# Kernel optimization log

Hardware: AMD Instinct MI355X
Metric: run time of the kernel (lower is better)

The kernel has to match this reference:

```python
import jax, jax.numpy as jnp
import numpy as np

D_MODEL = 2048
N_HEADS = 32
N_KV = 8
HEAD_DIM = D_MODEL // N_HEADS  # 64
D_FF = 8192
ROPE_BASE = 10000.0
EPS = 1e-5
B, S = 2, 2048


def setup_inputs() -> dict:
    key = jax.random.key(0)
    ks = jax.random.split(key, 8)
    s = 0.02
    qkv_out = (N_HEADS + 2 * N_KV) * HEAD_DIM
    return {
        "x": jax.random.normal(ks[0], (B, S, D_MODEL), jnp.float32),
        "w_norm1": jnp.ones((D_MODEL,), jnp.float32),
        "w_qkv": jax.random.normal(ks[1], (D_MODEL, qkv_out), jnp.float32) * s,
        "w_out": jax.random.normal(ks[2], (D_MODEL, D_MODEL), jnp.float32) * s,
        "w_norm2": jnp.ones((D_MODEL,), jnp.float32),
        "w_gate": jax.random.normal(ks[3], (D_MODEL, D_FF), jnp.float32) * s,
        "w_up": jax.random.normal(ks[4], (D_MODEL, D_FF), jnp.float32) * s,
        "w_down": jax.random.normal(ks[5], (D_FF, D_MODEL), jnp.float32) * s,
    }


def _rmsnorm(x, w):
    var = jnp.mean(x * x, axis=-1, keepdims=True)
    return x * jax.lax.rsqrt(var + EPS) * w


def _rope(x, cos, sin):
    # x: [b, s, h, d]; cos/sin: [s, d/2]; non-interleaved (NeoX half split)
    half = x.shape[-1] // 2
    x1, x2 = x[..., :half], x[..., half:]
    c = cos[None, :, None, :]
    sn = sin[None, :, None, :]
    return jnp.concatenate([x1 * c - x2 * sn, x1 * sn + x2 * c], axis=-1)


def _forward(x, w_norm1, w_qkv, w_out, w_norm2, w_gate, w_up, w_down):
    b, s, d = x.shape
    # --- attention block ---
    h = _rmsnorm(x, w_norm1)
    qkv = h @ w_qkv  # [b, s, (H + 2*KV) * hd]
    q = qkv[..., : N_HEADS * HEAD_DIM].reshape(b, s, N_HEADS, HEAD_DIM)
    kv = qkv[..., N_HEADS * HEAD_DIM:].reshape(b, s, 2, N_KV, HEAD_DIM)
    k, v = kv[:, :, 0], kv[:, :, 1]

    inv_freq = 1.0 / (ROPE_BASE ** (jnp.arange(0, HEAD_DIM, 2, dtype=jnp.float32) / HEAD_DIM))
    t = jnp.arange(s, dtype=jnp.float32)
    freqs = t[:, None] * inv_freq[None, :]  # [s, hd/2]
    cos, sin = jnp.cos(freqs), jnp.sin(freqs)
    q = _rope(q, cos, sin)
    k = _rope(k, cos, sin)

    # GQA: repeat_interleave kv heads to match q heads
    g = N_HEADS // N_KV
    k = jnp.repeat(k, g, axis=2)  # [b, s, H, hd]
    v = jnp.repeat(v, g, axis=2)

    scale = 1.0 / np.sqrt(HEAD_DIM)
    scores = jnp.einsum("bqhd,bkhd->bhqk", q, k) * scale
    causal = jnp.tril(jnp.ones((s, s), bool))
    scores = jnp.where(causal[None, None], scores, jnp.finfo(scores.dtype).min)
    attn = jax.nn.softmax(scores, axis=-1)
    ctx = jnp.einsum("bhqk,bkhd->bqhd", attn, v).reshape(b, s, N_HEADS * HEAD_DIM)
    x = x + ctx @ w_out

    # --- MLP block (SwiGLU) ---
    h2 = _rmsnorm(x, w_norm2)
    mlp = (jax.nn.silu(h2 @ w_gate) * (h2 @ w_up)) @ w_down
    return x + mlp


def reference(x, w_norm1, w_qkv, w_out, w_norm2, w_gate, w_up, w_down):
    return _forward(x, w_norm1, w_qkv, w_out, w_norm2, w_gate, w_up, w_down)
```

## Files before the change

### kernel.cpp

```cpp
#include <hip/hip_runtime.h>
#include <stdint.h>

#define D_MODEL 2048
#define S_LEN   2048
#define NTOK    4096
#define QKV_N   3072
#define DFF     8192

typedef float  f32x4   __attribute__((ext_vector_type(4)));
typedef float  f32x16  __attribute__((ext_vector_type(16)));
typedef __bf16 bf16x8  __attribute__((ext_vector_type(8)));
typedef unsigned short u16;
typedef unsigned short u16x8 __attribute__((ext_vector_type(8)));

__device__ __forceinline__ float b2f(u16 u){ union{float f; uint32_t i;} v; v.i = ((uint32_t)u) << 16; return v.f; }
__device__ __forceinline__ u16 f2b(float f){
  union{float f; uint32_t i;} v; v.f = f;
  uint32_t r = v.i + 0x7FFFu + ((v.i >> 16) & 1u);
  return (u16)(r >> 16);
}

__device__ __forceinline__ void gload_lds16(const void* gsrc, void* ldst){
  __builtin_amdgcn_global_load_lds(
      (const __attribute__((address_space(1))) void*)gsrc,
      (__attribute__((address_space(3))) void*)ldst,
      16, 0, 0);
}

__global__ __launch_bounds__(256) void wconv_kernel(const float* __restrict__ W, u16* __restrict__ WT,
                                                    int Nfull, int Kt, int Nt, int k0g, int n0g)
{
  __shared__ float tile[64][65];
  const int nTn = Nt >> 6;
  const int tk = blockIdx.x / nTn, tn = blockIdx.x % nTn;
  const int k0 = tk << 6, n0 = tn << 6;
  const int t  = threadIdx.x;
  const int c4 = (t & 15) << 2;
  const int r  = t >> 4;
#pragma unroll
  for (int i = 0; i < 4; ++i) {
    float4 v = *reinterpret_cast<const float4*>(&W[(size_t)(k0g + k0 + r + i*16) * Nfull + n0g + n0 + c4]);
    tile[r + i*16][c4+0] = v.x; tile[r + i*16][c4+1] = v.y;
    tile[r + i*16][c4+2] = v.z; tile[r + i*16][c4+3] = v.w;
  }
  __syncthreads();
#pragma unroll
  for (int i = 0; i < 4; ++i) {
    int n = r + i*16;
    ushort4 ov;
    ov.x = f2b(tile[c4+0][n]); ov.y = f2b(tile[c4+1][n]);
    ov.z = f2b(tile[c4+2][n]); ov.w = f2b(tile[c4+3][n]);
    *reinterpret_cast<ushort4*>(&WT[(size_t)(n0 + n) * Kt + k0 + c4]) = ov;
  }
}

__global__ void sincos_kernel(float* __restrict__ ct, float* __restrict__ st)
{
  int idx = blockIdx.x * 256 + threadIdx.x;
  if (idx >= S_LEN * 32) return;
  int p = idx >> 5, i = idx & 31;
  double freq = pow(10000.0, -((double)(2*i)) / 64.0);
  double ang  = (double)p * freq;
  ct[idx] = (float)cos(ang);
  st[idx] = (float)sin(ang);
}

template<bool BF16IN>
__global__ __launch_bounds__(256) void rmsnorm_kernel(const void* __restrict__ xin, const float* __restrict__ w, u16* __restrict__ out)
{
  const int row = blockIdx.x;
  const int t = threadIdx.x;
  float v[8];
  if (BF16IN) {
    const u16* xr = ((const u16*)xin) + (size_t)row * D_MODEL;
    u16x8 a = *reinterpret_cast<const u16x8*>(&xr[t*8]);
#pragma unroll
    for (int j = 0; j < 8; ++j) v[j] = b2f(a[j]);
  } else {
    const float* xr = ((const float*)xin) + (size_t)row * D_MODEL;
    float4 a = *reinterpret_cast<const float4*>(&xr[t*8]);
    float4 c = *reinterpret_cast<const float4*>(&xr[t*8+4]);
    v[0]=a.x; v[1]=a.y; v[2]=a.z; v[3]=a.w; v[4]=c.x; v[5]=c.y; v[6]=c.z; v[7]=c.w;
  }
  float ss = 0.f;
#pragma unroll
  for (int j = 0; j < 8; ++j) ss += v[j]*v[j];
#pragma unroll
  for (int d = 1; d < 64; d <<= 1) ss += __shfl_xor(ss, d);
  __shared__ float red[4];
  if ((t & 63) == 0) red[t >> 6] = ss;
  __syncthreads();
  ss = red[0] + red[1] + red[2] + red[3];
  const float sc = rsqrtf(ss * (1.0f / (float)D_MODEL) + 1e-5f);
  float4 w0 = *reinterpret_cast<const float4*>(&w[t*8]);
  float4 w1 = *reinterpret_cast<const float4*>(&w[t*8+4]);
  u16x8 o;
  o[0]=f2b(v[0]*sc*w0.x); o[1]=f2b(v[1]*sc*w0.y); o[2]=f2b(v[2]*sc*w0.z); o[3]=f2b(v[3]*sc*w0.w);
  o[4]=f2b(v[4]*sc*w1.x); o[5]=f2b(v[5]*sc*w1.y); o[6]=f2b(v[6]*sc*w1.z); o[7]=f2b(v[7]*sc*w1.w);
  *reinterpret_cast<u16x8*>(&out[(size_t)row * D_MODEL + t*8]) = o;
}

template<int EPI>
__device__ __forceinline__ void epi_store(size_t idx, float v, float* Cf, u16* Cb,
                                          const float* resf, const u16* resb, const u16* other)
{
  if (EPI == 2)      Cb[idx] = f2b(v / (1.0f + __expf(-v)));
  else if (EPI == 3) Cb[idx] = f2b(v * b2f(other[idx]));
  else if (EPI == 4) Cb[idx] = f2b(v);
  else if (EPI == 5) Cf[idx] += v;
  else if (EPI == 6) Cb[idx] = f2b(v + resf[idx]);
  else if (EPI == 7) Cf[idx] = v + b2f(resb[idx]);
}

template<int EPI>
__global__ __launch_bounds__(512, 2) void gemm8p_kernel(
    const u16* __restrict__ A, const u16* __restrict__ BT,
    int K, int lda, int ldb, int ldc, int n_off,
    float* Cf, u16* Cb,
    const float* __restrict__ resf, const u16* __restrict__ resb, const u16* other)
{
  __shared__ u16 lds[65536];
  const int tid = threadIdx.x;
  const int w = tid >> 6, lane = tid & 63;
  const int g = lane >> 4, lr = lane & 15;
  const int wm = w >> 2, wn = w & 3;
  const int bn = blockIdx.x, bm = blockIdx.y;
  const int NT = K >> 6;
  const int NI = NT >> 1;

  const int srow = tid >> 3;
  const int sg   = (tid & 7) ^ (srow & 7);
  const u16* Asrc = A  + (size_t)(bm * 256) * lda;
  const u16* Bsrc = BT + (size_t)(bn * 256) * ldb;

  const int agc0 = ((0 + g) ^ (lr & 7)) * 8;
  const int agc1 = ((4 + g) ^ (lr & 7)) * 8;

  f32x4 acc[8][4];
#pragma unroll
  for (int i = 0; i < 8; ++i)
#pragma unroll
    for (int j = 0; j < 4; ++j) acc[i][j] = (f32x4){0.f, 0.f, 0.f, 0.f};
  bf16x8 af[4][2], bf0[2][2], bf1[2][2];

#define STAGE_H(isB, h, b, T) do {                                           \
    int tc = ((T) < NT) ? (T) : (NT - 1);                                    \
    const u16* sb = (isB) ? Bsrc : Asrc;                                     \
    const int  sld = (isB) ? ldb : lda;                                      \
    const u16* s0 = sb + (size_t)((h)*128 + srow) * sld + tc*64 + sg*8;      \
    u16* dst = &lds[(b)*32768 + (isB)*16384 + (h)*8192 + tid*8];             \
    gload_lds16(s0, dst);                                                    \
    gload_lds16(s0 + (size_t)64 * sld, dst + 4096);                          \
  } while (0)

#define LOADA(mih, b) { _Pragma("unroll") for (int q = 0; q < 4; ++q) {      \
    const u16* rp = &lds[(b)*32768 + (wm*128 + (mih)*64 + q*16 + lr) * 64];  \
    af[q][0] = *(const bf16x8*)(rp + agc0);                                  \
    af[q][1] = *(const bf16x8*)(rp + agc1); } }

#define LOADB(dst, nih, b) { _Pragma("unroll") for (int nq = 0; nq < 2; ++nq) { \
    const u16* rp = &lds[(b)*32768 + 16384 + (wn*64 + (nih)*32 + nq*16 + lr) * 64]; \
    dst[nq][0] = *(const bf16x8*)(rp + agc0);                                \
    dst[nq][1] = *(const bf16x8*)(rp + agc1); } }

#define MM(mih, nih, BF) {                                                   \
    __builtin_amdgcn_s_setprio(1);                                           \
    _Pragma("unroll") for (int kk = 0; kk < 2; ++kk)                         \
      _Pragma("unroll") for (int q = 0; q < 4; ++q)                          \
        _Pragma("unroll") for (int nq = 0; nq < 2; ++nq)                     \
          acc[(mih)*4+q][(nih)*2+nq] = __builtin_amdgcn_mfma_f32_16x16x32_bf16( \
              af[q][kk], BF[nq][kk], acc[(mih)*4+q][(nih)*2+nq], 0, 0, 0);   \
    __builtin_amdgcn_s_setprio(0); }

#define SYNC_MID  __builtin_amdgcn_s_barrier();                              \
                  asm volatile("s_waitcnt lgkmcnt(0)" ::: "memory");         \
                  __builtin_amdgcn_sched_barrier(0);
#define PHEND     __builtin_amdgcn_s_barrier();
#define PHEND_VM  asm volatile("s_waitcnt vmcnt(4)" ::: "memory");           \
                  __builtin_amdgcn_s_barrier();

  STAGE_H(0, 0, 0, 0); STAGE_H(0, 1, 0, 0);
  STAGE_H(1, 0, 0, 0); STAGE_H(1, 1, 0, 0);
  STAGE_H(1, 0, 1, 1); STAGE_H(1, 1, 1, 1);
  asm volatile("s_waitcnt vmcnt(4)" ::: "memory");
  __builtin_amdgcn_s_barrier();

  for (int i = 0; i < NI; ++i) {
    const int t0 = 2 * i;
    LOADA(0, 0); LOADB(bf0, 0, 0);
    STAGE_H(0, 0, 1, t0 + 1);
    SYNC_MID; MM(0, 0, bf0); PHEND;
    LOADB(bf1, 1, 0);
    STAGE_H(0, 1, 1, t0 + 1);
    SYNC_MID; MM(0, 1, bf1); PHEND;
    LOADA(1, 0);
    STAGE_H(1, 0, 0, t0 + 2);
    SYNC_MID; MM(1, 1, bf1); PHEND;
    STAGE_H(1, 1, 0, t0 + 2);
    SYNC_MID; MM(1, 0, bf0); PHEND_VM;
    LOADA(0, 1); LOADB(bf0, 0, 1);
    STAGE_H(0, 0, 0, t0 + 2);
    SYNC_MID; MM(0, 0, bf0); PHEND;
    LOADB(bf1, 1, 1);
    STAGE_H(0, 1, 0, t0 + 2);
    SYNC_MID; MM(0, 1, bf1); PHEND;
    LOADA(1, 1);
    STAGE_H(1, 0, 1, t0 + 3);
    SYNC_MID; MM(1, 1, bf1); PHEND;
    STAGE_H(1, 1, 1, t0 + 3);
    SYNC_MID; MM(1, 0, bf0); PHEND_VM;
  }
#undef STAGE_H
#undef LOADA
#undef LOADB
#undef MM

#pragma unroll
  for (int mi = 0; mi < 8; ++mi) {
    const int rowOff = (mi >> 2) * 64 + (mi & 3) * 16;
#pragma unroll
    for (int ni = 0; ni < 4; ++ni) {
      const int colOff = (ni >> 1) * 32 + (ni & 1) * 16;
#pragma unroll
      for (int j = 0; j < 4; ++j) {
        int row = bm*256 + wm*128 + rowOff + g*4 + j;
        int col = n_off + bn*256 + wn*64 + colOff + lr;
        epi_store<EPI>((size_t)row * ldc + col, acc[mi][ni][j], Cf, Cb, resf, resb, other);
      }
    }
  }
}

template<int EPI>
__global__ __launch_bounds__(512) void gemm128_kernel(
    const u16* __restrict__ A, const u16* __restrict__ BT,
    int K, int lda, int ldb, int ldc, int n_off,
    float* Cf, u16* Cb,
    const float* __restrict__ resf, const u16* __restrict__ resb, const u16* other)
{
  __shared__ u16 lds[49152];
  const int tid = threadIdx.x;
  const int w = tid >> 6, lane = tid & 63;
  const int g = lane >> 4, lr = lane & 15;
  const int wm = w >> 2, wn = w & 3;
  const int bn = blockIdx.x, bm = blockIdx.y;
  const int NT = K >> 6;
  const int NI = NT >> 1;

  const int srow = tid >> 3;
  const int sg   = (tid & 7) ^ (srow & 7);
  const u16* Asrc = A  + (size_t)(bm * 128) * lda;
  const u16* Bsrc = BT + (size_t)(bn * 256) * ldb;

  const int agc0 = ((0 + g) ^ (lr & 7)) * 8;
  const int agc1 = ((4 + g) ^ (lr & 7)) * 8;

  f32x4 acc[4][4];
#pragma unroll
  for (int i = 0; i < 4; ++i)
#pragma unroll
    for (int j = 0; j < 4; ++j) acc[i][j] = (f32x4){0.f, 0.f, 0.f, 0.f};
  bf16x8 af[2][2], bf0[2][2], bf1[2][2];

#define STAGE_A(b, T) do {                                                   \
    int tc = ((T) < NT) ? (T) : (NT - 1);                                    \
    const u16* s0 = Asrc + (size_t)srow * lda + tc*64 + sg*8;                \
    u16* dst = &lds[(b)*24576 + tid*8];                                      \
    gload_lds16(s0, dst);                                                    \
    gload_lds16(s0 + (size_t)64 * lda, dst + 4096);                          \
  } while (0)

#define STAGE_BH(h, b, T) do {                                               \
    int tc = ((T) < NT) ? (T) : (NT - 1);                                    \
    const u16* s0 = Bsrc + (size_t)((h)*128 + srow) * ldb + tc*64 + sg*8;    \
    u16* dst = &lds[(b)*24576 + 8192 + (h)*8192 + tid*8];                    \
    gload_lds16(s0, dst);                                                    \
    gload_lds16(s0 + (size_t)64 * ldb, dst + 4096);                         \
  } while (0)

#define LOADA(mih, b) { _Pragma("unroll") for (int q = 0; q < 2; ++q) {      \
    const u16* rp = &lds[(b)*24576 + (wm*64 + (mih)*32 + q*16 + lr) * 64];   \
    af[q][0] = *(const bf16x8*)(rp + agc0);                                  \
    af[q][1] = *(const bf16x8*)(rp + agc1); } }

#define LOADB(dst, nih, b) { _Pragma("unroll") for (int nq = 0; nq < 2; ++nq) { \
    const u16* rp = &lds[(b)*24576 + 8192 + (wn*64 + (nih)*32 + nq*16 + lr) * 64]; \
    dst[nq][0] = *(const bf16x8*)(rp + agc0);                                \
    dst[nq][1] = *(const bf16x8*)(rp + agc1); } }

#define MM(mih, nih, BF) {                                                   \
    __builtin_amdgcn_s_setprio(1);                                           \
    _Pragma("unroll") for (int kk = 0; kk < 2; ++kk)                         \
      _Pragma("unroll") for (int q = 0; q < 2; ++q)                          \
        _Pragma("unroll") for (int nq = 0; nq < 2; ++nq)                     \
          acc[(mih)*2+q][(nih)*2+nq] = __builtin_amdgcn_mfma_f32_16x16x32_bf16( \
              af[q][kk], BF[nq][kk], acc[(mih)*2+q][(nih)*2+nq], 0, 0, 0);   \
    __builtin_amdgcn_s_setprio(0); }

  STAGE_A(0, 0); STAGE_BH(0, 0, 0); STAGE_BH(1, 0, 0);
  STAGE_BH(0, 1, 1); STAGE_BH(1, 1, 1);
  asm volatile("s_waitcnt vmcnt(4)" ::: "memory");
  __builtin_amdgcn_s_barrier();

  for (int i = 0; i < NI; ++i) {
    const int t0 = 2 * i;
    LOADA(0, 0); LOADB(bf0, 0, 0);
    STAGE_A(1, t0 + 1);
    SYNC_MID; MM(0, 0, bf0); PHEND;
    LOADB(bf1, 1, 0);
    STAGE_BH(0, 0, t0 + 2);
    SYNC_MID; MM(0, 1, bf1); PHEND;
    LOADA(1, 0);
    STAGE_BH(1, 0, t0 + 2);
    SYNC_MID; MM(1, 1, bf1); PHEND;
    STAGE_A(0, t0 + 2);
    SYNC_MID; MM(1, 0, bf0);
    asm volatile("s_waitcnt vmcnt(6)" ::: "memory");
    __builtin_amdgcn_s_barrier();
    LOADA(0, 1); LOADB(bf0, 0, 1);
    SYNC_MID; MM(0, 0, bf0); PHEND;
    LOADB(bf1, 1, 1);
    STAGE_BH(0, 1, t0 + 3);
    SYNC_MID; MM(0, 1, bf1); PHEND;
    LOADA(1, 1);
    STAGE_BH(1, 1, t0 + 3);
    SYNC_MID; MM(1, 1, bf1); PHEND;
    SYNC_MID; MM(1, 0, bf0);
    asm volatile("s_waitcnt vmcnt(4)" ::: "memory");
    __builtin_amdgcn_s_barrier();
  }
#undef STAGE_A
#undef STAGE_BH
#undef LOADA
#undef LOADB
#undef MM
#undef SYNC_MID
#undef PHEND
#undef PHEND_VM

#pragma unroll
  for (int mi = 0; mi < 4; ++mi) {
    const int rowOff = (mi >> 1) * 32 + (mi & 1) * 16;
#pragma unroll
    for (int ni = 0; ni < 4; ++ni) {
      const int colOff = (ni >> 1) * 32 + (ni & 1) * 16;
#pragma unroll
      for (int j = 0; j < 4; ++j) {
        int row = bm*128 + wm*64 + rowOff + g*4 + j;
        int col = n_off + bn*256 + wn*64 + colOff + lr;
        epi_store<EPI>((size_t)row * ldc + col, acc[mi][ni][j], Cf, Cb, resf, resb, other);
      }
    }
  }
}

__global__ __launch_bounds__(256) void rope_kernel(
    const u16* __restrict__ qkv, const float* __restrict__ ct, const float* __restrict__ st,
    u16* __restrict__ Q, u16* __restrict__ Kt, u16* __restrict__ VT)
{
  const int tok = blockIdx.x;
  const int b = tok >> 11, s = tok & (S_LEN - 1);
  const int w = threadIdx.x >> 6, lane = threadIdx.x & 63;
  const size_t base = (size_t)tok * QKV_N;
  for (int slot = w; slot < 48; slot += 4) {
    int col = (slot < 32) ? slot * 64 : (slot < 40 ? 2048 + (slot - 32) * 64 : 2560 + (slot - 40) * 64);
    float v = b2f(qkv[base + col + lane]);
    if (slot < 40) {
      int i = lane & 31;
      float c = ct[s * 32 + i], sn = st[s * 32 + i];
      float p = b2f(qkv[base + col + (lane ^ 32)]);
      v = (lane < 32) ? (v * c - p * sn) : (v * c + p * sn);
    }
    u16 ob = f2b(v);
    if (slot < 32)      Q [((size_t)(b * 32 + slot)      * S_LEN + s) * 64 + lane] = ob;
    else if (slot < 40) Kt[((size_t)(b * 8 + slot - 32)  * S_LEN + s) * 64 + lane] = ob;
    else                VT[((size_t)(b * 8 + slot - 40)  * 64 + lane) * S_LEN + s] = ob;
  }
}

#define ASCALE 0.1803368801111204f
__global__ __launch_bounds__(256, 3) void attn_kernel(
    const u16* __restrict__ Q, const u16* __restrict__ Kt,
    const u16* __restrict__ VT, u16* __restrict__ ctx,
    u16* __restrict__ po, float2* __restrict__ pml)
{
  const int bh  = blockIdx.x;
  const int y   = blockIdx.y;
  int qb, split;
  if (y < 16) { qb = 15 - (y >> 1); split = y & 1; }
  else        { qb = 23 - y;        split = -1;    }
  const int wid = threadIdx.x >> 6;
  const int lane = threadIdx.x & 63;
  const int b = bh >> 5, h = bh & 31;
  const int kvh = (b << 3) + (h >> 2);
  const int q0 = qb * 128 + wid * 32;
  const int cq = lane & 31;
  const int hi = lane >> 5;

  const u16* Qb = Q  + ((size_t)bh * S_LEN + q0) * 64;
  const u16* Kb = Kt + (size_t)kvh * S_LEN * 64;
  const u16* Vb = VT + (size_t)kvh * 64 * S_LEN;

  bf16x8 qf[4];
#pragma unroll
  for (int t = 0; t < 4; ++t)
    qf[t] = *reinterpret_cast<const bf16x8*>(&Qb[cq * 64 + t * 16 + hi * 8]);

  f32x16 o0 = {}, o1 = {};
  float m = -1e30f, l = 0.f;

  __shared__ float xch[4][32];

  const int nt = qb * 4 + wid + 1;
  const int ts = (split == 1) ? (nt >> 1) : 0;
  const int te = (split == 0) ? (nt >> 1) : nt;

  for (int t = ts; t < te; ++t) {
    const int k0 = t << 5;
    bf16x8 kf[4], vf[4];
#pragma unroll
    for (int tt = 0; tt < 4; ++tt)
      kf[tt] = *reinterpret_cast<const bf16x8*>(&Kb[(size_t)(k0 + cq) * 64 + tt * 16 + hi * 8]);
#pragma unroll
    for (int kh = 0; kh < 2; ++kh)
#pragma unroll
      for (int dh = 0; dh < 2; ++dh)
        vf[kh * 2 + dh] = *reinterpret_cast<const bf16x8*>(&Vb[(size_t)(dh * 32 + cq) * S_LEN + k0 + kh * 16 + hi * 8]);

    f32x16 sA = {}, sB = {};
    sA = __builtin_amdgcn_mfma_f32_32x32x16_bf16(kf[0], qf[0], sA, 0, 0, 0);
    sB = __builtin_amdgcn_mfma_f32_32x32x16_bf16(kf[1], qf[1], sB, 0, 0, 0);
    sA = __builtin_amdgcn_mfma_f32_32x32x16_bf16(kf[2], qf[2], sA, 0, 0, 0);
    sB = __builtin_amdgcn_mfma_f32_32x32x16_bf16(kf[3], qf[3], sB, 0, 0, 0);

    float p[16];
#pragma unroll
    for (int r = 0; r < 16; ++r) p[r] = (sA[r] + sB[r]) * ASCALE;
    if (t == nt - 1) {
#pragma unroll
      for (int r = 0; r < 16; ++r) {
        int kk = (r & 3) + 8 * (r >> 2) + 4 * hi;
        if (kk > cq) p[r] = -1e30f;
      }
    }
    float tmax = p[0];
#pragma unroll
    for (int r = 1; r < 16; ++r) tmax = fmaxf(tmax, p[r]);
    tmax = fmaxf(tmax, __shfl_xor(tmax, 32));

    if (!__all(tmax <= m + 8.0f)) {
      float mn = fmaxf(m, tmax);
      float corr = exp2f(m - mn);
      m = mn;
      l *= corr;
      if (hi == 0) xch[wid][cq] = corr;
      asm volatile("s_waitcnt lgkmcnt(0)" ::: "memory");
      __builtin_amdgcn_sched_barrier(0);
      float4 c0 = *reinterpret_cast<const float4*>(&xch[wid][4 * hi + 0]);
      float4 c1 = *reinterpret_cast<const float4*>(&xch[wid][4 * hi + 8]);
      float4 c2 = *reinterpret_cast<const float4*>(&xch[wid][4 * hi + 16]);
      float4 c3 = *reinterpret_cast<const float4*>(&xch[wid][4 * hi + 24]);
      float ca[16] = {c0.x,c0.y,c0.z,c0.w, c1.x,c1.y,c1.z,c1.w,
                      c2.x,c2.y,c2.z,c2.w, c3.x,c3.y,c3.z,c3.w};
#pragma unroll
      for (int r = 0; r < 16; ++r) { o0[r] *= ca[r]; o1[r] *= ca[r]; }
    }

    float tsum = 0.f;
#pragma unroll
    for (int r = 0; r < 16; ++r) { p[r] = exp2f(p[r] - m); tsum += p[r]; }
    tsum += __shfl_xor(tsum, 32);
    l += tsum;

    uint32_t wds[8], pw[8];
#pragma unroll
    for (int j = 0; j < 8; ++j) {
      uint32_t wv;
      asm("v_cvt_pk_bf16_f32 %0, %1, %2" : "=v"(wv) : "v"(p[2*j]), "v"(p[2*j+1]));
      wds[j] = wv;
    }
#pragma unroll
    for (int j = 0; j < 8; ++j) pw[j] = __shfl_xor(wds[j], 32);
    union { uint32_t u[4]; bf16x8 v; } pa0, pa1;
    pa0.u[0] = hi ? pw[2]  : wds[0];
    pa0.u[1] = hi ? pw[3]  : wds[1];
    pa0.u[2] = hi ? wds[2] : pw[0];
    pa0.u[3] = hi ? wds[3] : pw[1];
    pa1.u[0] = hi ? pw[6]  : wds[4];
    pa1.u[1] = hi ? pw[7]  : wds[5];
    pa1.u[2] = hi ? wds[6] : pw[4];
    pa1.u[3] = hi ? wds[7] : pw[5];

    o0 = __builtin_amdgcn_mfma_f32_32x32x16_bf16(pa0.v, vf[0], o0, 0, 0, 0);
    o0 = __builtin_amdgcn_mfma_f32_32x32x16_bf16(pa1.v, vf[2], o0, 0, 0, 0);
    o1 = __builtin_amdgcn_mfma_f32_32x32x16_bf16(pa0.v, vf[1], o1, 0, 0, 0);
    o1 = __builtin_amdgcn_mfma_f32_32x32x16_bf16(pa1.v, vf[3], o1, 0, 0, 0);
  }

  if (split < 0) {
    float linv = 1.0f / l;
    if (hi == 0) xch[wid][cq] = linv;
    asm volatile("s_waitcnt lgkmcnt(0)" ::: "memory");
    __builtin_amdgcn_sched_barrier(0);
    float4 n0 = *reinterpret_cast<const float4*>(&xch[wid][4 * hi + 0]);
    float4 n1 = *reinterpret_cast<const float4*>(&xch[wid][4 * hi + 8]);
    float4 n2 = *reinterpret_cast<const float4*>(&xch[wid][4 * hi + 16]);
    float4 n3 = *reinterpret_cast<const float4*>(&xch[wid][4 * hi + 24]);
    float na[16] = {n0.x,n0.y,n0.z,n0.w, n1.x,n1.y,n1.z,n1.w,
                    n2.x,n2.y,n2.z,n2.w, n3.x,n3.y,n3.z,n3.w};
#pragma unroll
    for (int r = 0; r < 16; ++r) {
      int row = (r & 3) + 8 * (r >> 2) + 4 * hi;
      size_t base = (size_t)(b * S_LEN + q0 + row) * D_MODEL + h * 64;
      ctx[base + cq]      = f2b(o0[r] * na[r]);
      ctx[base + 32 + cq] = f2b(o1[r] * na[r]);
    }
  } else {
    const int qr0 = q0 - 1024;
    if (hi == 0) {
      float2 v; v.x = m; v.y = l;
      pml[((size_t)(split * 64 + bh)) * 1024 + qr0 + cq] = v;
    }
#pragma unroll
    for (int r = 0; r < 16; ++r) {
      int row = (r & 3) + 8 * (r >> 2) + 4 * hi;
      size_t base = (((size_t)(split * 64 + bh)) * 1024 + qr0 + row) * 64;
      po[base + cq]      = f2b(o0[r]);
      po[base + 32 + cq] = f2b(o1[r]);
    }
  }
}

__global__ __launch_bounds__(256) void attn_combine(
    const u16* __restrict__ po, const float2* __restrict__ pml, u16* __restrict__ ctx)
{
  const int bh = blockIdx.x;
  const int b = bh >> 5, h = bh & 31;
  const int d = threadIdx.x & 63;
  for (int rr = threadIdx.x >> 6; rr < 64; rr += 4) {
    const int qr = blockIdx.y * 64 + rr;
    float2 ml1 = pml[(size_t)bh * 1024 + qr];
    float2 ml2 = pml[(size_t)(64 + bh) * 1024 + qr];
    float mm = fmaxf(ml1.x, ml2.x);
    float w1 = exp2f(ml1.x - mm), w2 = exp2f(ml2.x - mm);
    float denom = ml1.y * w1 + ml2.y * w2;
    float v1 = b2f(po[((size_t)bh * 1024 + qr) * 64 + d]);
    float v2 = b2f(po[((size_t)(64 + bh) * 1024 + qr) * 64 + d]);
    ctx[((size_t)(b * S_LEN) + 1024 + qr) * D_MODEL + h * 64 + d] = f2b((v1 * w1 + v2 * w2) / denom);
  }
}

extern "C" void kernel_launch(void* const* d_in, const int* in_sizes, int n_in,
                              void* d_out, int out_size, void* d_ws, size_t ws_size,
                              hipStream_t stream)
{
  const float* x     = (const float*)d_in[0];
  const float* wn1   = (const float*)d_in[1];
  const float* wqkv  = (const float*)d_in[2];
  const float* wout  = (const float*)d_in[3];
  const float* wn2   = (const float*)d_in[4];
  const float* wgate = (const float*)d_in[5];
  const float* wup   = (const float*)d_in[6];
  const float* wdown = (const float*)d_in[7];
  float* out = (float*)d_out;
  char* ws = (char*)d_ws;

  float* cosT = (float*)(ws + 0);
  float* sinT = (float*)(ws + 262144);
  u16*   wT   = (u16*)  (ws + 524288);
  u16*   hB   = (u16*)  (ws + 17301504);
  u16*   x1b  = (u16*)  (ws + 34078720);
  char*  S    = ws + 50855936;
  u16*   qkvB = (u16*)(S + 0);
  u16*   poB  = (u16*)(S + 0);
  float2* pmlB= (float2*)(S + 16777216);
  u16*   qB   = (u16*)(S + 25165824);
  u16*   kB   = (u16*)(S + 41943040);
  u16*   vtB  = (u16*)(S + 46137344);
  u16*   ctxB = (u16*)(S + 50331648);
  u16*   gsB  = (u16*)(S + 0);

  sincos_kernel<<<dim3(256), 256, 0, stream>>>(cosT, sinT);
  rmsnorm_kernel<false><<<dim3(NTOK), 256, 0, stream>>>(x, wn1, hB);

  wconv_kernel<<<dim3((2048/64)*(3072/64)), 256, 0, stream>>>(wqkv, wT, 3072, 2048, 3072, 0, 0);
  gemm128_kernel<4><<<dim3(QKV_N/256, NTOK/128), 512, 0, stream>>>(hB, wT, 2048, 2048, 2048, 3072, 0, nullptr, qkvB, nullptr, nullptr, nullptr);
  rope_kernel<<<dim3(NTOK), 256, 0, stream>>>(qkvB, cosT, sinT, qB, kB, vtB);
  attn_kernel<<<dim3(64, 24), 256, 0, stream>>>(qB, kB, vtB, ctxB, poB, pmlB);
  attn_combine<<<dim3(64, 16), 256, 0, stream>>>(poB, pmlB, ctxB);

  wconv_kernel<<<dim3((2048/64)*(2048/64)), 256, 0, stream>>>(wout, wT, 2048, 2048, 2048, 0, 0);
  gemm128_kernel<6><<<dim3(D_MODEL/256, NTOK/128), 512, 0, stream>>>(ctxB, wT, 2048, 2048, 2048, 2048, 0, nullptr, x1b, x, nullptr, nullptr);

  rmsnorm_kernel<true><<<dim3(NTOK), 256, 0, stream>>>(x1b, wn2, hB);

  for (int c = 0; c < 2; ++c) {
    wconv_kernel<<<dim3((2048/64)*(4096/64)), 256, 0, stream>>>(wgate, wT, 8192, 2048, 4096, 0, c*4096);
    gemm8p_kernel<2><<<dim3(4096/256, NTOK/256), 512, 0, stream>>>(hB, wT, 2048, 2048, 2048, 8192, c*4096, nullptr, gsB, nullptr, nullptr, nullptr);
  }
  for (int c = 0; c < 2; ++c) {
    wconv_kernel<<<dim3((2048/64)*(4096/64)), 256, 0, stream>>>(wup, wT, 8192, 2048, 4096, 0, c*4096);
    gemm8p_kernel<3><<<dim3(4096/256, NTOK/256), 512, 0, stream>>>(hB, wT, 2048, 2048, 2048, 8192, c*4096, nullptr, gsB, nullptr, nullptr, gsB);
  }
  wconv_kernel<<<dim3((4096/64)*(2048/64)), 256, 0, stream>>>(wdown, wT, 2048, 4096, 2048, 0, 0);
  gemm128_kernel<7><<<dim3(D_MODEL/256, NTOK/128), 512, 0, stream>>>(gsB, wT, 4096, 8192, 4096, 2048, 0, out, nullptr, nullptr, x1b, nullptr);
  wconv_kernel<<<dim3((4096/64)*(2048/64)), 256, 0, stream>>>(wdown, wT, 2048, 4096, 2048, 4096, 0);
  gemm128_kernel<5><<<dim3(D_MODEL/256, NTOK/128), 512, 0, stream>>>(gsB + 4096, wT, 4096, 8192, 4096, 2048, 0, out, nullptr, nullptr, nullptr, nullptr);
}
```

Measured before the change: 826.4 us.

## Drop attention split-K and combine; double-buffer K loads in attention loop

Removes the two-way KV split for the later query blocks along with the separate combine kernel and its partial-output buffers, so every query block is handled by a single workgroup. The inner loop now double-buffers K fragments, prefetching the next tile while the current one is computed, and it hoists the K/V pointer arithmetic out of the loop. The per-tile row-sum shuffle is deferred to one reduction at the end. The aim is to cut the combine launch and the partial-result memory traffic and to hide K load latency, at the cost of longer, less balanced tail workgroups and more registers.

Result: no change. 811.8 us (-1.8%).

```diff
diff --git a/kernel.cpp b/kernel.cpp
--- a/kernel.cpp
+++ b/kernel.cpp
@@ -381,14 +381,10 @@
 #define ASCALE 0.1803368801111204f
 __global__ __launch_bounds__(256, 3) void attn_kernel(
     const u16* __restrict__ Q, const u16* __restrict__ Kt,
-    const u16* __restrict__ VT, u16* __restrict__ ctx,
-    u16* __restrict__ po, float2* __restrict__ pml)
+    const u16* __restrict__ VT, u16* __restrict__ ctx)
 {
   const int bh  = blockIdx.x;
-  const int y   = blockIdx.y;
-  int qb, split;
-  if (y < 16) { qb = 15 - (y >> 1); split = y & 1; }
-  else        { qb = 23 - y;        split = -1;    }
+  const int qb  = 15 - blockIdx.y;
   const int wid = threadIdx.x >> 6;
   const int lane = threadIdx.x & 63;
   const int b = bh >> 5, h = bh & 31;
@@ -398,8 +394,12 @@
   const int hi = lane >> 5;
 
   const u16* Qb = Q  + ((size_t)bh * S_LEN + q0) * 64;
-  const u16* Kb = Kt + (size_t)kvh * S_LEN * 64;
-  const u16* Vb = VT + (size_t)kvh * 64 * S_LEN;
+  const u16* Kp = Kt + (size_t)kvh * S_LEN * 64 + cq * 64 + hi * 8;
+  const u16* Vbase = VT + (size_t)kvh * 64 * S_LEN + hi * 8;
+  const u16* Vp[4];
+#pragma unroll
+  for (int v = 0; v < 4; ++v)
+    Vp[v] = Vbase + (size_t)((v & 1) * 32 + cq) * S_LEN + (v >> 1) * 16;
 
   bf16x8 qf[4];
 #pragma unroll
@@ -412,141 +412,107 @@
   __shared__ float xch[4][32];
 
   const int nt = qb * 4 + wid + 1;
-  const int ts = (split == 1) ? (nt >> 1) : 0;
-  const int te = (split == 0) ? (nt >> 1) : nt;
-
-  for (int t = ts; t < te; ++t) {
-    const int k0 = t << 5;
-    bf16x8 kf[4], vf[4];
-#pragma unroll
-    for (int tt = 0; tt < 4; ++tt)
-      kf[tt] = *reinterpret_cast<const bf16x8*>(&Kb[(size_t)(k0 + cq) * 64 + tt * 16 + hi * 8]);
-#pragma unroll
-    for (int kh = 0; kh < 2; ++kh)
-#pragma unroll
-      for (int dh = 0; dh < 2; ++dh)
-        vf[kh * 2 + dh] = *reinterpret_cast<const bf16x8*>(&Vb[(size_t)(dh * 32 + cq) * S_LEN + k0 + kh * 16 + hi * 8]);
-
-    f32x16 sA = {}, sB = {};
-    sA = __builtin_amdgcn_mfma_f32_32x32x16_bf16(kf[0], qf[0], sA, 0, 0, 0);
-    sB = __builtin_amdgcn_mfma_f32_32x32x16_bf16(kf[1], qf[1], sB, 0, 0, 0);
-    sA = __builtin_amdgcn_mfma_f32_32x32x16_bf16(kf[2], qf[2], sA, 0, 0, 0);
-    sB = __builtin_amdgcn_mfma_f32_32x32x16_bf16(kf[3], qf[3], sB, 0, 0, 0);
-
-    float p[16];
-#pragma unroll
-    for (int r = 0; r < 16; ++r) p[r] = (sA[r] + sB[r]) * ASCALE;
-    if (t == nt - 1) {
-#pragma unroll
-      for (int r = 0; r < 16; ++r) {
-        int kk = (r & 3) + 8 * (r >> 2) + 4 * hi;
-        if (kk > cq) p[r] = -1e30f;
-      }
-    }
-    float tmax = p[0];
-#pragma unroll
-    for (int r = 1; r < 16; ++r) tmax = fmaxf(tmax, p[r]);
-    tmax = fmaxf(tmax, __shfl_xor(tmax, 32));
-
-    if (!__all(tmax <= m + 8.0f)) {
-      float mn = fmaxf(m, tmax);
-      float corr = exp2f(m - mn);
-      m = mn;
-      l *= corr;
-      if (hi == 0) xch[wid][cq] = corr;
-      asm volatile("s_waitcnt lgkmcnt(0)" ::: "memory");
-      __builtin_amdgcn_sched_barrier(0);
-      float4 c0 = *reinterpret_cast<const float4*>(&xch[wid][4 * hi + 0]);
-      float4 c1 = *reinterpret_cast<const float4*>(&xch[wid][4 * hi + 8]);
-      float4 c2 = *reinterpret_cast<const float4*>(&xch[wid][4 * hi + 16]);
-      float4 c3 = *reinterpret_cast<const float4*>(&xch[wid][4 * hi + 24]);
-      float ca[16] = {c0.x,c0.y,c0.z,c0.w, c1.x,c1.y,c1.z,c1.w,
-                      c2.x,c2.y,c2.z,c2.w, c3.x,c3.y,c3.z,c3.w};
-#pragma unroll
-      for (int r = 0; r < 16; ++r) { o0[r] *= ca[r]; o1[r] *= ca[r]; }
-    }
-
-    float tsum = 0.f;
-#pragma unroll
-    for (int r = 0; r < 16; ++r) { p[r] = exp2f(p[r] - m); tsum += p[r]; }
-    tsum += __shfl_xor(tsum, 32);
-    l += tsum;
-
-    uint32_t wds[8], pw[8];
-#pragma unroll
-    for (int j = 0; j < 8; ++j) {
-      uint32_t wv;
-      asm("v_cvt_pk_bf16_f32 %0, %1, %2" : "=v"(wv) : "v"(p[2*j]), "v"(p[2*j+1]));
-      wds[j] = wv;
-    }
-#pragma unroll
-    for (int j = 0; j < 8; ++j) pw[j] = __shfl_xor(wds[j], 32);
-    union { uint32_t u[4]; bf16x8 v; } pa0, pa1;
-    pa0.u[0] = hi ? pw[2]  : wds[0];
-    pa0.u[1] = hi ? pw[3]  : wds[1];
-    pa0.u[2] = hi ? wds[2] : pw[0];
-    pa0.u[3] = hi ? wds[3] : pw[1];
-    pa1.u[0] = hi ? pw[6]  : wds[4];
-    pa1.u[1] = hi ? pw[7]  : wds[5];
-    pa1.u[2] = hi ? wds[6] : pw[4];
-    pa1.u[3] = hi ? wds[7] : pw[5];
-
-    o0 = __builtin_amdgcn_mfma_f32_32x32x16_bf16(pa0.v, vf[0], o0, 0, 0, 0);
-    o0 = __builtin_amdgcn_mfma_f32_32x32x16_bf16(pa1.v, vf[2], o0, 0, 0, 0);
-    o1 = __builtin_amdgcn_mfma_f32_32x32x16_bf16(pa0.v, vf[1], o1, 0, 0, 0);
-    o1 = __builtin_amdgcn_mfma_f32_32x32x16_bf16(pa1.v, vf[3], o1, 0, 0, 0);
-  }
-
-  if (split < 0) {
-    float linv = 1.0f / l;
-    if (hi == 0) xch[wid][cq] = linv;
-    asm volatile("s_waitcnt lgkmcnt(0)" ::: "memory");
-    __builtin_amdgcn_sched_barrier(0);
-    float4 n0 = *reinterpret_cast<const float4*>(&xch[wid][4 * hi + 0]);
-    float4 n1 = *reinterpret_cast<const float4*>(&xch[wid][4 * hi + 8]);
-    float4 n2 = *reinterpret_cast<const float4*>(&xch[wid][4 * hi + 16]);
-    float4 n3 = *reinterpret_cast<const float4*>(&xch[wid][4 * hi + 24]);
-    float na[16] = {n0.x,n0.y,n0.z,n0.w, n1.x,n1.y,n1.z,n1.w,
-                    n2.x,n2.y,n2.z,n2.w, n3.x,n3.y,n3.z,n3.w};
-#pragma unroll
-    for (int r = 0; r < 16; ++r) {
-      int row = (r & 3) + 8 * (r >> 2) + 4 * hi;
-      size_t base = (size_t)(b * S_LEN + q0 + row) * D_MODEL + h * 64;
-      ctx[base + cq]      = f2b(o0[r] * na[r]);
-      ctx[base + 32 + cq] = f2b(o1[r] * na[r]);
-    }
-  } else {
-    const int qr0 = q0 - 1024;
-    if (hi == 0) {
-      float2 v; v.x = m; v.y = l;
-      pml[((size_t)(split * 64 + bh)) * 1024 + qr0 + cq] = v;
-    }
-#pragma unroll
-    for (int r = 0; r < 16; ++r) {
-      int row = (r & 3) + 8 * (r >> 2) + 4 * hi;
-      size_t base = (((size_t)(split * 64 + bh)) * 1024 + qr0 + row) * 64;
-      po[base + cq]      = f2b(o0[r]);
-      po[base + 32 + cq] = f2b(o1[r]);
-    }
-  }
-}
-
-__global__ __launch_bounds__(256) void attn_combine(
-    const u16* __restrict__ po, const float2* __restrict__ pml, u16* __restrict__ ctx)
-{
-  const int bh = blockIdx.x;
-  const int b = bh >> 5, h = bh & 31;
-  const int d = threadIdx.x & 63;
-  for (int rr = threadIdx.x >> 6; rr < 64; rr += 4) {
-    const int qr = blockIdx.y * 64 + rr;
-    float2 ml1 = pml[(size_t)bh * 1024 + qr];
-    float2 ml2 = pml[(size_t)(64 + bh) * 1024 + qr];
-    float mm = fmaxf(ml1.x, ml2.x);
-    float w1 = exp2f(ml1.x - mm), w2 = exp2f(ml2.x - mm);
-    float denom = ml1.y * w1 + ml2.y * w2;
-    float v1 = b2f(po[((size_t)bh * 1024 + qr) * 64 + d]);
-    float v2 = b2f(po[((size_t)(64 + bh) * 1024 + qr) * 64 + d]);
-    ctx[((size_t)(b * S_LEN) + 1024 + qr) * D_MODEL + h * 64 + d] = f2b((v1 * w1 + v2 * w2) / denom);
+
+#define ATT_LOADK(KF, T) { _Pragma("unroll") for (int q_ = 0; q_ < 4; ++q_) \
+    KF[q_] = *(const bf16x8*)(Kp + (T) * 2048 + q_ * 16); }
+#define ATT_LOADV(VF, T) { _Pragma("unroll") for (int v_ = 0; v_ < 4; ++v_) \
+    VF[v_] = *(const bf16x8*)(Vp[v_] + (T) * 32); }
+
+#define ATT_COMPUTE(KF, VF, T) do {                                          \
+    f32x16 sA = {}, sB = {};                                                 \
+    sA = __builtin_amdgcn_mfma_f32_32x32x16_bf16(KF[0], qf[0], sA, 0, 0, 0); \
+    sB = __builtin_amdgcn_mfma_f32_32x32x16_bf16(KF[1], qf[1], sB, 0, 0, 0); \
+    sA = __builtin_amdgcn_mfma_f32_32x32x16_bf16(KF[2], qf[2], sA, 0, 0, 0); \
+    sB = __builtin_amdgcn_mfma_f32_32x32x16_bf16(KF[3], qf[3], sB, 0, 0, 0); \
+    float p[16];                                                             \
+    _Pragma("unroll") for (int r = 0; r < 16; ++r) p[r] = (sA[r] + sB[r]) * ASCALE; \
+    if ((T) == nt - 1) {                                                     \
+      _Pragma("unroll") for (int r = 0; r < 16; ++r) {                       \
+        int kk = (r & 3) + 8 * (r >> 2) + 4 * hi;                            \
+        if (kk > cq) p[r] = -1e30f;                                          \
+      }                                                                      \
+    }                                                                        \
+    float m0_ = fmaxf(fmaxf(p[0], p[1]), p[2]);                              \
+    float m1_ = fmaxf(fmaxf(p[3], p[4]), p[5]);                              \
+    float m2_ = fmaxf(fmaxf(p[6], p[7]), p[8]);                              \
+    float m3_ = fmaxf(fmaxf(p[9], p[10]), p[11]);                            \
+    float m4_ = fmaxf(fmaxf(p[12], p[13]), p[14]);                           \
+    float tmax = fmaxf(fmaxf(fmaxf(m0_, m1_), m2_), fmaxf(fmaxf(m3_, m4_), p[15])); \
+    tmax = fmaxf(tmax, __shfl_xor(tmax, 32));                                \
+    if (!__all(tmax <= m + 8.0f)) {                                          \
+      float mn = fmaxf(m, tmax);                                             \
+      float corr = exp2f(m - mn);                                            \
+      m = mn;                                                                \
+      l *= corr;                                                             \
+      if (hi == 0) xch[wid][cq] = corr;                                      \
+      asm volatile("s_waitcnt lgkmcnt(0)" ::: "memory");                     \
+      __builtin_amdgcn_sched_barrier(0);                                     \
+      float4 c0 = *reinterpret_cast<const float4*>(&xch[wid][4 * hi + 0]);   \
+      float4 c1 = *reinterpret_cast<const float4*>(&xch[wid][4 * hi + 8]);   \
+      float4 c2 = *reinterpret_cast<const float4*>(&xch[wid][4 * hi + 16]);  \
+      float4 c3 = *reinterpret_cast<const float4*>(&xch[wid][4 * hi + 24]);  \
+      float ca[16] = {c0.x,c0.y,c0.z,c0.w, c1.x,c1.y,c1.z,c1.w,              \
+                      c2.x,c2.y,c2.z,c2.w, c3.x,c3.y,c3.z,c3.w};             \
+      _Pragma("unroll") for (int r = 0; r < 16; ++r) { o0[r] *= ca[r]; o1[r] *= ca[r]; } \
+    }                                                                        \
+    float tsum = 0.f;                                                        \
+    _Pragma("unroll") for (int r = 0; r < 16; ++r) { p[r] = exp2f(p[r] - m); tsum += p[r]; } \
+    l += tsum;                                                               \
+    uint32_t wds[8], pw[8];                                                  \
+    _Pragma("unroll") for (int j = 0; j < 8; ++j) {                          \
+      uint32_t wv;                                                           \
+      asm("v_cvt_pk_bf16_f32 %0, %1, %2" : "=v"(wv) : "v"(p[2*j]), "v"(p[2*j+1])); \
+      wds[j] = wv;                                                           \
+    }                                                                        \
+    _Pragma("unroll") for (int j = 0; j < 8; ++j) pw[j] = __shfl_xor(wds[j], 32); \
+    union { uint32_t u[4]; bf16x8 v; } pa0, pa1;                             \
+    pa0.u[0] = hi ? pw[2]  : wds[0];                                         \
+    pa0.u[1] = hi ? pw[3]  : wds[1];                                         \
+    pa0.u[2] = hi ? wds[2] : pw[0];                                          \
+    pa0.u[3] = hi ? wds[3] : pw[1];                                          \
+    pa1.u[0] = hi ? pw[6]  : wds[4];                                         \
+    pa1.u[1] = hi ? pw[7]  : wds[5];                                         \
+    pa1.u[2] = hi ? wds[6] : pw[4];                                          \
+    pa1.u[3] = hi ? wds[7] : pw[5];                                          \
+    o0 = __builtin_amdgcn_mfma_f32_32x32x16_bf16(pa0.v, VF[0], o0, 0, 0, 0); \
+    o0 = __builtin_amdgcn_mfma_f32_32x32x16_bf16(pa1.v, VF[2], o0, 0, 0, 0); \
+    o1 = __builtin_amdgcn_mfma_f32_32x32x16_bf16(pa0.v, VF[1], o1, 0, 0, 0); \
+    o1 = __builtin_amdgcn_mfma_f32_32x32x16_bf16(pa1.v, VF[3], o1, 0, 0, 0); \
+  } while (0)
+
+  bf16x8 kf0[4], kf1[4], vf[4];
+  ATT_LOADK(kf0, 0);
+  for (int t = 0; t < nt; ) {
+    if (t + 1 < nt) ATT_LOADK(kf1, t + 1);
+    ATT_LOADV(vf, t);
+    ATT_COMPUTE(kf0, vf, t);
+    ++t; if (t >= nt) break;
+    if (t + 1 < nt) ATT_LOADK(kf0, t + 1);
+    ATT_LOADV(vf, t);
+    ATT_COMPUTE(kf1, vf, t);
+    ++t;
+  }
+#undef ATT_LOADK
+#undef ATT_LOADV
+#undef ATT_COMPUTE
+
+  l += __shfl_xor(l, 32);
+  float linv = 1.0f / l;
+  if (hi == 0) xch[wid][cq] = linv;
+  asm volatile("s_waitcnt lgkmcnt(0)" ::: "memory");
+  __builtin_amdgcn_sched_barrier(0);
+  float4 n0 = *reinterpret_cast<const float4*>(&xch[wid][4 * hi + 0]);
+  float4 n1 = *reinterpret_cast<const float4*>(&xch[wid][4 * hi + 8]);
+  float4 n2 = *reinterpret_cast<const float4*>(&xch[wid][4 * hi + 16]);
+  float4 n3 = *reinterpret_cast<const float4*>(&xch[wid][4 * hi + 24]);
+  float na[16] = {n0.x,n0.y,n0.z,n0.w, n1.x,n1.y,n1.z,n1.w,
+                  n2.x,n2.y,n2.z,n2.w, n3.x,n3.y,n3.z,n3.w};
+#pragma unroll
+  for (int r = 0; r < 16; ++r) {
+    int row = (r & 3) + 8 * (r >> 2) + 4 * hi;
+    size_t base = (size_t)(b * S_LEN + q0 + row) * D_MODEL + h * 64;
+    ctx[base + cq]      = f2b(o0[r] * na[r]);
+    ctx[base + 32 + cq] = f2b(o1[r] * na[r]);
   }
 }
 
@@ -572,8 +538,6 @@
   u16*   x1b  = (u16*)  (ws + 34078720);
   char*  S    = ws + 50855936;
   u16*   qkvB = (u16*)(S + 0);
-  u16*   poB  = (u16*)(S + 0);
-  float2* pmlB= (float2*)(S + 16777216);
   u16*   qB   = (u16*)(S + 25165824);
   u16*   kB   = (u16*)(S + 41943040);
   u16*   vtB  = (u16*)(S + 46137344);
@@ -586,8 +550,7 @@
   wconv_kernel<<<dim3((2048/64)*(3072/64)), 256, 0, stream>>>(wqkv, wT, 3072, 2048, 3072, 0, 0);
   gemm128_kernel<4><<<dim3(QKV_N/256, NTOK/128), 512, 0, stream>>>(hB, wT, 2048, 2048, 2048, 3072, 0, nullptr, qkvB, nullptr, nullptr, nullptr);
   rope_kernel<<<dim3(NTOK), 256, 0, stream>>>(qkvB, cosT, sinT, qB, kB, vtB);
-  attn_kernel<<<dim3(64, 24), 256, 0, stream>>>(qB, kB, vtB, ctxB, poB, pmlB);
-  attn_combine<<<dim3(64, 16), 256, 0, stream>>>(poB, pmlB, ctxB);
+  attn_kernel<<<dim3(64, 16), 256, 0, stream>>>(qB, kB, vtB, ctxB);
 
   wconv_kernel<<<dim3((2048/64)*(2048/64)), 256, 0, stream>>>(wout, wT, 2048, 2048, 2048, 0, 0);
   gemm128_kernel<6><<<dim3(D_MODEL/256, NTOK/128), 512, 0, stream>>>(ctxB, wT, 2048, 2048, 2048, 2048, 0, nullptr, x1b, x, nullptr, nullptr);
```
